# Kernel optimization log

Hardware: AMD Instinct MI355X
Metric: run time of the kernel (lower is better)

## Reference

```python
import jax, jax.numpy as jnp
import numpy as np

N = 50000   # num_nodes
E = 300000  # num_edges
D = 256     # args.dim
F = 1024    # feat_dim
C = 40      # num_labels

def setup_inputs() -> dict:
    key = jax.random.key(0)
    ks = jax.random.split(key, 16)
    def lin(k, fan_in, shape):
        return (jax.random.normal(k, shape, jnp.float32) / np.float32(np.sqrt(fan_in)))
    return {
        "feat": jax.random.normal(ks[0], (N, F), jnp.float32),
        "src": jax.random.randint(ks[1], (E,), 0, N, dtype=jnp.int32),
        "dst": jax.random.randint(ks[2], (E,), 0, N, dtype=jnp.int32),
        "W_fc": lin(ks[3], F, (F, D)), "b_fc": jnp.zeros((D,), jnp.float32),
        "W1": lin(ks[4], D, (D, D)), "b1": jnp.zeros((D,), jnp.float32),
        "W2": lin(ks[5], D, (D, D)), "b2": jnp.zeros((D,), jnp.float32),
        "W3": lin(ks[6], D, (D, D)), "b3": jnp.zeros((D,), jnp.float32),
        "gamma": jnp.ones((D,), jnp.float32), "beta": jnp.zeros((D,), jnp.float32),
        "W_lin": lin(ks[7], D, (D, C)), "b_lin": jnp.zeros((C,), jnp.float32),
    }

def _norms(src, dst, n):
    # DGL GraphConv norm='both': out-degree norm on src side, in-degree on dst side, clamp(min=1)
    ones = jnp.ones(src.shape[0], jnp.float32)
    deg_out = jnp.clip(jax.ops.segment_sum(ones, src, num_segments=n), 1.0)
    deg_in = jnp.clip(jax.ops.segment_sum(ones, dst, num_segments=n), 1.0)
    return deg_out[:, None] ** -0.5, deg_in[:, None] ** -0.5

def _gconv(x, src, dst, norm_s, norm_d, W, b):
    h = x * norm_s                              # [N, D]
    m = jax.ops.segment_sum(h[src], dst, num_segments=x.shape[0])  # SpMM via gather/scatter
    return (m * norm_d) @ W + b

def _bn_elu(x, gamma, beta):
    # training-mode batchnorm math (batch stats, biased var); dropout is identity (eval)
    mu = x.mean(axis=0)
    var = x.var(axis=0)
    y = gamma * (x - mu) * jax.lax.rsqrt(var + 1e-5) + beta
    return jax.nn.elu(y)

def reference(feat, src, dst, W_fc, b_fc, W1, b1, W2, b2, W3, b3, gamma, beta, W_lin, b_lin):
    norm_s, norm_d = _norms(src, dst, feat.shape[0])
    x = feat @ W_fc + b_fc
    x = _gconv(x, src, dst, norm_s, norm_d, W1, b1)
    x = _bn_elu(x, gamma, beta)
    x = _gconv(x, src, dst, norm_s, norm_d, W2, b2)
    x = _bn_elu(x, gamma, beta)
    x = _gconv(x, src, dst, norm_s, norm_d, W3, b3)
    return (x, x @ W_lin + b_lin)
```

## Files before the change

### kernel.cpp

```cpp
#include <hip/hip_runtime.h>

#define N_NODES 50000
#define N_EDGES 300000
#define DIM 256
#define FEAT 1024
#define NCLS 40

typedef unsigned short u16;
typedef __attribute__((ext_vector_type(8))) short short8;
typedef __attribute__((ext_vector_type(4))) float float4v;

__device__ __forceinline__ float bf2f(u16 u) {
  union { float f; unsigned v; } x; x.v = ((unsigned)u) << 16; return x.f;
}
__device__ __forceinline__ u16 f2bf(float f) {
  union { float f; unsigned v; } x; x.f = f;
  unsigned r = 0x7fffu + ((x.v >> 16) & 1u);
  return (u16)((x.v + r) >> 16);
}
__device__ __forceinline__ float flexload(const void* p, size_t i, int f32) {
  return f32 ? ((const float*)p)[i] : bf2f(((const u16*)p)[i]);
}
__device__ __forceinline__ void flexstore(void* p, size_t i, int f32, float v) {
  if (f32) ((float*)p)[i] = v;
  else ((u16*)p)[i] = f2bf(v);
}
__device__ __forceinline__ void async16(const u16* g, u16* l) {
  __builtin_amdgcn_global_load_lds(
      (__attribute__((address_space(1))) void*)g,
      (__attribute__((address_space(3))) void*)l, 16, 0, 0);
}

__global__ __launch_bounds__(256) void k_sniff(const u16* __restrict__ feat,
                                               int* __restrict__ dflag) {
  __shared__ int cnt[256];
  int t = threadIdx.x;
  int ok = 0;
  for (int j = 0; j < 4; ++j) {
    float v = bf2f(feat[(size_t)(t * 4 + j) * 2]);
    float a = fabsf(v);
    if (a < 64.0f && a > 1e-5f) ok++;
  }
  cnt[t] = ok;
  __syncthreads();
  for (int off = 128; off > 0; off >>= 1) {
    if (t < off) cnt[t] += cnt[t + off];
    __syncthreads();
  }
  if (t == 0) dflag[0] = (cnt[0] < 700) ? 1 : 0;
}

__global__ void k_setflag(int* dflag, int v) { dflag[0] = v; }

__global__ void k_filldiag(void* out, int n, float val, const int* __restrict__ dflag) {
  int i = blockIdx.x * blockDim.x + threadIdx.x;
  if (i < n) flexstore(out, i, dflag[0], val);
}

__global__ __launch_bounds__(256) void k_cast(const void* __restrict__ feat,
                                              u16* __restrict__ xf,
                                              const int* __restrict__ dflag) {
  if (dflag[0] == 0) return;
  size_t i = ((size_t)blockIdx.x * 256 + threadIdx.x) * 8;
  const float* f = (const float*)feat;
  float4 a = *(const float4*)&f[i];
  float4 b = *(const float4*)&f[i + 4];
  uint4 o;
  o.x = (unsigned)f2bf(a.x) | ((unsigned)f2bf(a.y) << 16);
  o.y = (unsigned)f2bf(a.z) | ((unsigned)f2bf(a.w) << 16);
  o.z = (unsigned)f2bf(b.x) | ((unsigned)f2bf(b.y) << 16);
  o.w = (unsigned)f2bf(b.z) | ((unsigned)f2bf(b.w) << 16);
  *(uint4*)&xf[i] = o;
}


__global__ void k_zero(unsigned* p, int n) {
  int i = blockIdx.x * blockDim.x + threadIdx.x;
  if (i < n) p[i] = 0u;
}

__global__ void k_deg(const int* __restrict__ src, const int* __restrict__ dst,
                      float* __restrict__ degf, int* __restrict__ degi, int e) {
  int i = blockIdx.x * blockDim.x + threadIdx.x;
  if (i < e) {
    atomicAdd(&degf[src[i]], 1.0f);
    atomicAdd(&degi[dst[i]], 1);
  }
}

__global__ void k_norm(const float* __restrict__ degf, const int* __restrict__ degi,
                       float* __restrict__ ns, float* __restrict__ nd, int n) {
  int i = blockIdx.x * blockDim.x + threadIdx.x;
  if (i < n) {
    ns[i] = rsqrtf(fmaxf(degf[i], 1.0f));
    nd[i] = rsqrtf(fmaxf((float)degi[i], 1.0f));
  }
}

__global__ __launch_bounds__(1024) void k_scan(const int* __restrict__ counts,
                                               int* __restrict__ row_start,
                                               int* __restrict__ cursor, int n) {
  __shared__ int wsum[16];
  __shared__ int carry_s;
  int t = threadIdx.x;
  int lane = t & 63, wv = t >> 6;
  if (t == 0) carry_s = 0;
  __syncthreads();
  for (int base = 0; base < n; base += 4096) {
    int i0 = base + t * 4;
    int v0 = 0, v1 = 0, v2 = 0, v3 = 0;
    if (i0 + 3 < n) {
      int4 c4 = *(const int4*)&counts[i0];
      v0 = c4.x; v1 = c4.y; v2 = c4.z; v3 = c4.w;
    } else {
      if (i0 < n) v0 = counts[i0];
      if (i0 + 1 < n) v1 = counts[i0 + 1];
      if (i0 + 2 < n) v2 = counts[i0 + 2];
      if (i0 + 3 < n) v3 = counts[i0 + 3];
    }
    int s = v0 + v1 + v2 + v3;
    int sc = s;
#pragma unroll
    for (int off = 1; off < 64; off <<= 1) {
      int u = __shfl_up(sc, off, 64);
      if (lane >= off) sc += u;
    }
    if (lane == 63) wsum[wv] = sc;
    __syncthreads();
    if (wv == 0) {
      int w_ = (lane < 16) ? wsum[lane] : 0;
#pragma unroll
      for (int off = 1; off < 16; off <<= 1) {
        int u = __shfl_up(w_, off, 64);
        if (lane >= off) w_ += u;
      }
      if (lane < 16) wsum[lane] = w_;
    }
    __syncthreads();
    int wbase = (wv == 0) ? 0 : wsum[wv - 1];
    int carry = carry_s;
    int excl = carry + wbase + (sc - s);
    if (i0 < n)     { int p = excl;                row_start[i0] = p;     cursor[i0] = p; }
    if (i0 + 1 < n) { int p = excl + v0;           row_start[i0 + 1] = p; cursor[i0 + 1] = p; }
    if (i0 + 2 < n) { int p = excl + v0 + v1;      row_start[i0 + 2] = p; cursor[i0 + 2] = p; }
    if (i0 + 3 < n) { int p = excl + v0 + v1 + v2; row_start[i0 + 3] = p; cursor[i0 + 3] = p; }
    __syncthreads();
    if (t == 1023) carry_s = carry + wbase + sc;
    __syncthreads();
  }
  if (t == 0) row_start[n] = carry_s;
}

__global__ void k_scatter(const int* __restrict__ src, const int* __restrict__ dst,
                          int* __restrict__ cursor, int* __restrict__ csr_src, int e) {
  int i = blockIdx.x * blockDim.x + threadIdx.x;
  if (i < e) {
    int pos = atomicAdd(&cursor[dst[i]], 1);
    csr_src[pos] = src[i];
  }
}

__global__ void k_transpose(const void* __restrict__ w, u16* __restrict__ wt,
                            int K, int Ncols, const int* __restrict__ dflag) {
  int f = dflag[0];
  int i = blockIdx.x * blockDim.x + threadIdx.x;
  if (i < K * Ncols) {
    int k = i / Ncols;
    int c = i - k * Ncols;
    wt[c * K + k] = f2bf(flexload(w, i, f));
  }
}


__global__ __launch_bounds__(256) void k_gemm_a(
    const u16* __restrict__ A0, const u16* __restrict__ A1,
    const u16* __restrict__ Bt, const void* __restrict__ bias,
    void* __restrict__ Cmat, int M, int K, int Nc, int c_flex,
    float* __restrict__ stats, const int* __restrict__ dflag) {
  __shared__ __align__(16) u16 As[64 * 128];
  __shared__ __align__(16) u16 Bs[64 * 128];

  const int f = dflag[0];
  const u16* A = f ? A1 : A0;
  const int cf = c_flex & f;

  const int tid = threadIdx.x;
  const int lane = tid & 63;
  const int wv = tid >> 6;
  const int wm = (wv >> 1) * 64;
  const int wn = (wv & 1) * 64;
  const int quad = lane >> 4;
  const int l15 = lane & 15;
  const int rowBase = blockIdx.x * 128;
  const int colBase = blockIdx.y * 128;

  float4v acc[4][4];
#pragma unroll
  for (int a = 0; a < 4; ++a)
#pragma unroll
    for (int b = 0; b < 4; ++b) {
      acc[a][b][0] = 0.f; acc[a][b][1] = 0.f; acc[a][b][2] = 0.f; acc[a][b][3] = 0.f;
    }

  for (int k0 = 0; k0 < K; k0 += 64) {
    __syncthreads();
#pragma unroll
    for (int r = 0; r < 4; ++r) {
      int j = r * 256 + tid;
      int kq = j >> 7;
      int ml = j & 127;
      int grow = rowBase + ml;
      if (grow >= M) grow = M - 1;
      async16(&A[(size_t)grow * K + k0 + kq * 8], &As[j * 8]);
      async16(&Bt[(size_t)(colBase + ml) * K + k0 + kq * 8], &Bs[j * 8]);
    }
    __syncthreads();
#pragma unroll
    for (int ks = 0; ks < 2; ++ks) {
      short8 afr[4], bfr[4];
#pragma unroll
      for (int t = 0; t < 4; ++t) {
        int kq = ks * 4 + quad;
        afr[t] = *(const short8*)&As[(kq * 128 + wm + t * 16 + l15) * 8];
        bfr[t] = *(const short8*)&Bs[(kq * 128 + wn + t * 16 + l15) * 8];
      }
#pragma unroll
      for (int mt = 0; mt < 4; ++mt)
#pragma unroll
        for (int nt = 0; nt < 4; ++nt)
          acc[mt][nt] = __builtin_amdgcn_mfma_f32_16x16x32_bf16(
              afr[mt], bfr[nt], acc[mt][nt], 0, 0, 0);
    }
  }

#pragma unroll
  for (int nt = 0; nt < 4; ++nt) {
    int col = colBase + wn + nt * 16 + l15;
    float bv = flexload(bias, col, f);
    float s = 0.f, s2 = 0.f;
#pragma unroll
    for (int mt = 0; mt < 4; ++mt) {
#pragma unroll
      for (int r = 0; r < 4; ++r) {
        int row = rowBase + wm + mt * 16 + quad * 4 + r;
        if (row < M) {
          float v = acc[mt][nt][r] + bv;
          if (cf) ((float*)Cmat)[(size_t)row * Nc + col] = v;
          else ((u16*)Cmat)[(size_t)row * Nc + col] = f2bf(v);
          s += v;
          s2 += v * v;
        }
      }
    }
    if (stats) {
      s += __shfl_down(s, 32, 64);
      s += __shfl_down(s, 16, 64);
      s2 += __shfl_down(s2, 32, 64);
      s2 += __shfl_down(s2, 16, 64);
      if (quad == 0) {
        atomicAdd(&stats[col], s);
        atomicAdd(&stats[DIM + col], s2);
      }
    }
  }
}

__global__ __launch_bounds__(256) void k_gemm_flex(
    const void* __restrict__ A, const u16* __restrict__ Bt,
    const void* __restrict__ bias, void* __restrict__ Cmat,
    int M, int K, int Nc, int a_flex, int c_flex,
    const int* __restrict__ dflag) {
  __shared__ __align__(16) u16 As[64 * 128];
  __shared__ __align__(16) u16 Bs[64 * 128];
  const int f = dflag[0];
  const int af = a_flex & f;
  const int cf = c_flex & f;
  const int tid = threadIdx.x;
  const int lane = tid & 63;
  const int wv = tid >> 6;
  const int wm = (wv >> 1) * 64;
  const int wn = (wv & 1) * 64;
  const int quad = lane >> 4;
  const int l15 = lane & 15;
  const int rowBase = blockIdx.x * 128;
  const int colBase = blockIdx.y * 128;
  float4v acc[4][4];
#pragma unroll
  for (int a = 0; a < 4; ++a)
#pragma unroll
    for (int b = 0; b < 4; ++b) {
      acc[a][b][0] = 0.f; acc[a][b][1] = 0.f; acc[a][b][2] = 0.f; acc[a][b][3] = 0.f;
    }
  for (int k0 = 0; k0 < K; k0 += 64) {
    __syncthreads();
#pragma unroll
    for (int r = 0; r < 4; ++r) {
      int j = r * 256 + tid;
      int kq = j >> 7;
      int ml = j & 127;
      int grow = rowBase + ml;
      if (grow >= M) grow = M - 1;
      size_t abase = (size_t)grow * K + k0 + kq * 8;
      if (af) {
        const float* Af = (const float*)A;
        float4 lo = *(const float4*)&Af[abase];
        float4 hi = *(const float4*)&Af[abase + 4];
        u16* d = &As[j * 8];
        d[0] = f2bf(lo.x); d[1] = f2bf(lo.y); d[2] = f2bf(lo.z); d[3] = f2bf(lo.w);
        d[4] = f2bf(hi.x); d[5] = f2bf(hi.y); d[6] = f2bf(hi.z); d[7] = f2bf(hi.w);
      } else {
        const u16* Au = (const u16*)A;
        *(uint4*)&As[j * 8] = *(const uint4*)&Au[abase];
      }
      *(uint4*)&Bs[j * 8] = *(const uint4*)&Bt[(size_t)(colBase + ml) * K + k0 + kq * 8];
    }
    __syncthreads();
#pragma unroll
    for (int ks = 0; ks < 2; ++ks) {
      short8 afr[4], bfr[4];
#pragma unroll
      for (int t = 0; t < 4; ++t) {
        int kq = ks * 4 + quad;
        afr[t] = *(const short8*)&As[(kq * 128 + wm + t * 16 + l15) * 8];
        bfr[t] = *(const short8*)&Bs[(kq * 128 + wn + t * 16 + l15) * 8];
      }
#pragma unroll
      for (int mt = 0; mt < 4; ++mt)
#pragma unroll
        for (int nt = 0; nt < 4; ++nt)
          acc[mt][nt] = __builtin_amdgcn_mfma_f32_16x16x32_bf16(
              afr[mt], bfr[nt], acc[mt][nt], 0, 0, 0);
    }
  }
#pragma unroll
  for (int nt = 0; nt < 4; ++nt) {
    int col = colBase + wn + nt * 16 + l15;
    float bv = flexload(bias, col, f);
#pragma unroll
    for (int mt = 0; mt < 4; ++mt) {
#pragma unroll
      for (int r = 0; r < 4; ++r) {
        int row = rowBase + wm + mt * 16 + quad * 4 + r;
        if (row < M) {
          float v = acc[mt][nt][r] + bv;
          if (cf) ((float*)Cmat)[(size_t)row * Nc + col] = v;
          else ((u16*)Cmat)[(size_t)row * Nc + col] = f2bf(v);
        }
      }
    }
  }
}


__global__ __launch_bounds__(256) void k_spmm(
    const u16* __restrict__ x, u16* __restrict__ y,
    const int* __restrict__ row_start, const int* __restrict__ csr_src,
    const float* __restrict__ ns, const float* __restrict__ nd, int n) {
  int wid = (blockIdx.x * blockDim.x + threadIdx.x) >> 6;
  int lane = threadIdx.x & 63;
  if (wid >= n) return;
  int e0 = row_start[wid];
  int e1 = row_start[wid + 1];
  int c = lane * 4;
  float a0 = 0.f, a1 = 0.f, a2 = 0.f, a3 = 0.f;
  for (int e = e0; e < e1; ++e) {
    int s = csr_src[e];
    float w = ns[s];
    uint2 v = *(const uint2*)&x[(size_t)s * DIM + c];
    a0 += w * bf2f((u16)(v.x & 0xffffu));
    a1 += w * bf2f((u16)(v.x >> 16));
    a2 += w * bf2f((u16)(v.y & 0xffffu));
    a3 += w * bf2f((u16)(v.y >> 16));
  }
  float wd = nd[wid];
  uint2 o;
  o.x = (unsigned)f2bf(a0 * wd) | ((unsigned)f2bf(a1 * wd) << 16);
  o.y = (unsigned)f2bf(a2 * wd) | ((unsigned)f2bf(a3 * wd) << 16);
  *(uint2*)&y[(size_t)wid * DIM + c] = o;
}


__global__ __launch_bounds__(256) void k_bnfin(const float* __restrict__ stats,
                                               const void* __restrict__ gamma,
                                               const void* __restrict__ beta,
                                               float* __restrict__ gb, int nrows,
                                               const int* __restrict__ dflag) {
  int f = dflag[0];
  int t = threadIdx.x;
  float inv_n = 1.0f / (float)nrows;
  float mu = stats[t] * inv_n;
  float var = stats[DIM + t] * inv_n - mu * mu;
  float rs = rsqrtf(var + 1e-5f);
  float g = flexload(gamma, t, f) * rs;
  float b = flexload(beta, t, f) - mu * g;
  gb[t] = g;
  gb[DIM + t] = b;
}

__global__ __launch_bounds__(256) void k_bnapply(u16* __restrict__ x,
                                                 const float* __restrict__ gb, int nrows) {
  int t = threadIdx.x;
  float g = gb[t];
  float b = gb[DIM + t];
  for (int r = blockIdx.x; r < nrows; r += gridDim.x) {
    size_t idx = (size_t)r * DIM + t;
    float y = g * bf2f(x[idx]) + b;
    y = y > 0.f ? y : expm1f(y);
    x[idx] = f2bf(y);
  }
}


__global__ __launch_bounds__(256) void k_final(const void* __restrict__ x,
                                               const void* __restrict__ W,
                                               const void* __restrict__ bias,
                                               void* __restrict__ out, int nrows,
                                               const int* __restrict__ dflag) {
  __shared__ u16 xs[64 * DIM];
  __shared__ u16 wl[DIM * NCLS];
  int f = dflag[0];
  int t = threadIdx.x;
  int rowBase = blockIdx.x * 64;
  for (int i = t; i < 64 * DIM; i += 256) {
    int r = rowBase + (i >> 8);
    if (r >= nrows) r = nrows - 1;
    xs[i] = f2bf(flexload(x, (size_t)r * DIM + (i & 255), f));
  }
  for (int i = t; i < DIM * NCLS; i += 256) wl[i] = f2bf(flexload(W, i, f));
  __syncthreads();
  for (int o = t; o < 64 * NCLS; o += 256) {
    int r = o / NCLS;
    int c = o - r * NCLS;
    float acc = 0.f;
    const u16* xr = &xs[r * DIM];
#pragma unroll 8
    for (int k = 0; k < DIM; ++k) acc += bf2f(xr[k]) * bf2f(wl[k * NCLS + c]);
    int grow = rowBase + r;
    if (grow < nrows)
      flexstore(out, (size_t)N_NODES * DIM + (size_t)grow * NCLS + c, f,
                acc + flexload(bias, c, f));
  }
}


extern "C" void kernel_launch(void* const* d_in, const int* in_sizes, int n_in,
                              void* d_out, int out_size, void* d_ws, size_t ws_size,
                              hipStream_t stream) {
  static const int EXP[15] = {51200000, 300000, 300000, 262144, 256, 65536, 256,
                              65536, 256, 65536, 256, 256, 256, 10240, 40};
  bool ok_sizes = (n_in == 15);
  if (ok_sizes)
    for (int i = 0; i < 15; ++i)
      if (in_sizes[i] != EXP[i]) ok_sizes = false;

  char* w = (char*)d_ws;
  size_t o = 0;
  auto take = [&](size_t bytes) {
    size_t r = o;
    o += (bytes + 255) & ~(size_t)255;
    return r;
  };
  size_t o_degf = take(N_NODES * 4);
  size_t o_degi = take(N_NODES * 4);
  size_t o_stat = take(1024 * 4);
  size_t zero_bytes = o;
  size_t o_flag = take(256);
  size_t o_gb = take(512 * 4);
  size_t o_ns = take(N_NODES * 4);
  size_t o_nd = take(N_NODES * 4);
  size_t o_rs = take((N_NODES + 1) * 4);
  size_t o_cur = take(N_NODES * 4);
  size_t o_csr = take(N_EDGES * 4);
  size_t o_wfc = take((size_t)FEAT * DIM * 2);
  size_t o_w1 = take(DIM * DIM * 2);
  size_t o_w2 = take(DIM * DIM * 2);
  size_t o_w3 = take(DIM * DIM * 2);
  size_t o_xa = take((size_t)N_NODES * DIM * 2);
  size_t required = o;
  size_t o_xf = take((size_t)N_NODES * FEAT * 2);
  size_t required_xf = o;
  bool have_xf = ws_size >= required_xf;

  if (!ok_sizes || ws_size < required) {
    int* dflag0 = (int*)d_ws;
    float val = ok_sizes ? 1.0f : 2.0f;
    if (n_in > 0 && in_sizes[0] >= 2048)
      k_sniff<<<1, 256, 0, stream>>>((const u16*)d_in[0], dflag0);
    else
      k_setflag<<<1, 1, 0, stream>>>(dflag0, 0);
    k_filldiag<<<(out_size + 255) / 256, 256, 0, stream>>>(d_out, out_size, val, dflag0);
    return;
  }

  const void* feat = d_in[0];
  const int* src = (const int*)d_in[1];
  const int* dst = (const int*)d_in[2];
  const void* W_fc = d_in[3];
  const void* b_fc = d_in[4];
  const void* W1 = d_in[5];
  const void* b1 = d_in[6];
  const void* W2 = d_in[7];
  const void* b2 = d_in[8];
  const void* W3 = d_in[9];
  const void* b3 = d_in[10];
  const void* gamma = d_in[11];
  const void* beta = d_in[12];
  const void* W_lin = d_in[13];
  const void* b_lin = d_in[14];

  float* degf = (float*)(w + o_degf);
  int* degi = (int*)(w + o_degi);
  float* stats = (float*)(w + o_stat);
  int* dflag = (int*)(w + o_flag);
  float* gb = (float*)(w + o_gb);
  float* norm_s = (float*)(w + o_ns);
  float* norm_d = (float*)(w + o_nd);
  int* row_start = (int*)(w + o_rs);
  int* cursor = (int*)(w + o_cur);
  int* csr_src = (int*)(w + o_csr);
  u16* WtFc = (u16*)(w + o_wfc);
  u16* Wt1 = (u16*)(w + o_w1);
  u16* Wt2 = (u16*)(w + o_w2);
  u16* Wt3 = (u16*)(w + o_w3);
  u16* xA = (u16*)(w + o_xa);
  u16* xF = (u16*)(w + o_xf);

  u16* ping = (u16*)d_out;

  k_sniff<<<1, 256, 0, stream>>>((const u16*)feat, dflag);

  int zero_words = (int)(zero_bytes / 4);
  k_zero<<<(zero_words + 255) / 256, 256, 0, stream>>>((unsigned*)(w + 0), zero_words);
  k_deg<<<(N_EDGES + 255) / 256, 256, 0, stream>>>(src, dst, degf, degi, N_EDGES);
  k_norm<<<(N_NODES + 255) / 256, 256, 0, stream>>>(degf, degi, norm_s, norm_d, N_NODES);
  k_scan<<<1, 1024, 0, stream>>>(degi, row_start, cursor, N_NODES);
  k_scatter<<<(N_EDGES + 255) / 256, 256, 0, stream>>>(src, dst, cursor, csr_src, N_EDGES);
  k_transpose<<<((FEAT * DIM) + 255) / 256, 256, 0, stream>>>(W_fc, WtFc, FEAT, DIM, dflag);
  k_transpose<<<((DIM * DIM) + 255) / 256, 256, 0, stream>>>(W1, Wt1, DIM, DIM, dflag);
  k_transpose<<<((DIM * DIM) + 255) / 256, 256, 0, stream>>>(W2, Wt2, DIM, DIM, dflag);
  k_transpose<<<((DIM * DIM) + 255) / 256, 256, 0, stream>>>(W3, Wt3, DIM, DIM, dflag);

  dim3 gg((N_NODES + 127) / 128, DIM / 128);

  if (have_xf) {
    k_cast<<<(N_NODES * FEAT) / (256 * 8), 256, 0, stream>>>(feat, xF, dflag);
    k_gemm_a<<<gg, 256, 0, stream>>>((const u16*)feat, xF, WtFc, b_fc, ping,
                                     N_NODES, FEAT, DIM, 0, (float*)nullptr, dflag);
  } else {
    k_gemm_flex<<<gg, 256, 0, stream>>>(feat, WtFc, b_fc, ping,
                                        N_NODES, FEAT, DIM, 1, 0, dflag);
  }

  k_spmm<<<(N_NODES + 3) / 4, 256, 0, stream>>>(ping, xA, row_start, csr_src, norm_s, norm_d, N_NODES);
  k_gemm_a<<<gg, 256, 0, stream>>>(xA, xA, Wt1, b1, ping, N_NODES, DIM, DIM, 0, stats, dflag);
  k_bnfin<<<1, 256, 0, stream>>>(stats, gamma, beta, gb, N_NODES, dflag);
  k_bnapply<<<512, 256, 0, stream>>>(ping, gb, N_NODES);

  k_spmm<<<(N_NODES + 3) / 4, 256, 0, stream>>>(ping, xA, row_start, csr_src, norm_s, norm_d, N_NODES);
  k_gemm_a<<<gg, 256, 0, stream>>>(xA, xA, Wt2, b2, ping, N_NODES, DIM, DIM, 0, stats + 512, dflag);
  k_bnfin<<<1, 256, 0, stream>>>(stats + 512, gamma, beta, gb, N_NODES, dflag);
  k_bnapply<<<512, 256, 0, stream>>>(ping, gb, N_NODES);

  k_spmm<<<(N_NODES + 3) / 4, 256, 0, stream>>>(ping, xA, row_start, csr_src, norm_s, norm_d, N_NODES);
  k_gemm_a<<<gg, 256, 0, stream>>>(xA, xA, Wt3, b3, d_out, N_NODES, DIM, DIM, 1, (float*)nullptr, dflag);

  k_final<<<(N_NODES + 63) / 64, 256, 0, stream>>>(d_out, W_lin, b_lin, d_out, N_NODES, dflag);
}
```

Before: 1.010 ms.

## Fuse input cast into FC GEMM, fold BN-ELU into SpMM, precompose logits weights

Replaces the separate fp32-to-bf16 cast pass and tiled FC GEMM with one full-width kernel that loads fp32 features into LDS and converts them while building MFMA fragments. Folds the batchnorm+ELU apply into the next SpMM's gather, so the in-place normalise pass over activations goes away. Precomputes W3·W_lin and the combined bias, then computes logits with an MFMA kernel straight from the aggregated features instead of the scalar final kernel. In exchange, ELU is recomputed per gathered edge, rounding changes because the composed weight is stored in bf16, and the FC kernel uses more LDS and registers.

```diff
diff --git a/kernel.cpp b/kernel.cpp
--- a/kernel.cpp
+++ b/kernel.cpp
@@ -1,10 +1,12 @@
 #include <hip/hip_runtime.h>
+#include <hip/hip_bf16.h>
 
 #define N_NODES 50000
 #define N_EDGES 300000
 #define DIM 256
 #define FEAT 1024
 #define NCLS 40
+#define WPAD 264
 
 typedef unsigned short u16;
 typedef __attribute__((ext_vector_type(8))) short short8;
@@ -18,6 +20,11 @@
   unsigned r = 0x7fffu + ((x.v >> 16) & 1u);
   return (u16)((x.v + r) >> 16);
 }
+__device__ __forceinline__ unsigned pk2(float a, float b) {
+  union { __hip_bfloat162 h; unsigned u; } cv;
+  cv.h = __float22bfloat162_rn(make_float2(a, b));
+  return cv.u;
+}
 __device__ __forceinline__ float flexload(const void* p, size_t i, int f32) {
   return f32 ? ((const float*)p)[i] : bf2f(((const u16*)p)[i]);
 }
@@ -25,7 +32,7 @@
   if (f32) ((float*)p)[i] = v;
   else ((u16*)p)[i] = f2bf(v);
 }
-__device__ __forceinline__ void async16(const u16* g, u16* l) {
+__device__ __forceinline__ void async16(const void* g, void* l) {
   __builtin_amdgcn_global_load_lds(
       (__attribute__((address_space(1))) void*)g,
       (__attribute__((address_space(3))) void*)l, 16, 0, 0);
@@ -55,22 +62,6 @@
 __global__ void k_filldiag(void* out, int n, float val, const int* __restrict__ dflag) {
   int i = blockIdx.x * blockDim.x + threadIdx.x;
   if (i < n) flexstore(out, i, dflag[0], val);
-}
-
-__global__ __launch_bounds__(256) void k_cast(const void* __restrict__ feat,
-                                              u16* __restrict__ xf,
-                                              const int* __restrict__ dflag) {
-  if (dflag[0] == 0) return;
-  size_t i = ((size_t)blockIdx.x * 256 + threadIdx.x) * 8;
-  const float* f = (const float*)feat;
-  float4 a = *(const float4*)&f[i];
-  float4 b = *(const float4*)&f[i + 4];
-  uint4 o;
-  o.x = (unsigned)f2bf(a.x) | ((unsigned)f2bf(a.y) << 16);
-  o.y = (unsigned)f2bf(a.z) | ((unsigned)f2bf(a.w) << 16);
-  o.z = (unsigned)f2bf(b.x) | ((unsigned)f2bf(b.y) << 16);
-  o.w = (unsigned)f2bf(b.z) | ((unsigned)f2bf(b.w) << 16);
-  *(uint4*)&xf[i] = o;
 }
 
 
@@ -171,17 +162,147 @@
   }
 }
 
+__global__ __launch_bounds__(256) void k_combo(const void* __restrict__ W3,
+                                               const void* __restrict__ Wlin,
+                                               u16* __restrict__ Wct,
+                                               const int* __restrict__ dflag) {
+  int f = dflag[0];
+  int c = blockIdx.x;
+  int k = threadIdx.x;
+  float acc = 0.f;
+  if (c < NCLS)
+    for (int n = 0; n < DIM; ++n)
+      acc += flexload(W3, (size_t)k * DIM + n, f) * flexload(Wlin, (size_t)n * NCLS + c, f);
+  Wct[c * WPAD + k] = f2bf(acc);
+}
+
+__global__ void k_combobias(const void* __restrict__ b3, const void* __restrict__ Wlin,
+                            const void* __restrict__ blin, float* __restrict__ bcb,
+                            const int* __restrict__ dflag) {
+  int f = dflag[0];
+  int c = threadIdx.x;
+  if (c >= NCLS) return;
+  float acc = flexload(blin, c, f);
+  for (int n = 0; n < DIM; ++n)
+    acc += flexload(b3, n, f) * flexload(Wlin, (size_t)n * NCLS + c, f);
+  bcb[c] = acc;
+}
+
+
+__global__ __launch_bounds__(256) void k_gemm_fc(
+    const void* __restrict__ A, const u16* __restrict__ Bt,
+    const void* __restrict__ bias, u16* __restrict__ Cmat,
+    int M, const int* __restrict__ dflag) {
+  __shared__ __align__(16) u16 lds_[32768];
+  u16* Bs = lds_;
+  u16* Asb = lds_ + 16384;
+  float* Asf = (float*)(lds_ + 16384);
+
+  const int f = dflag[0];
+  const int tid = threadIdx.x;
+  const int lane = tid & 63;
+  const int wv = tid >> 6;
+  const int wm = (wv >> 1) * 64;
+  const int wn = (wv & 1) * 128;
+  const int quad = lane >> 4;
+  const int l15 = lane & 15;
+  const int rowBase = blockIdx.x * 128;
+
+  float4v acc[4][8];
+#pragma unroll
+  for (int a = 0; a < 4; ++a)
+#pragma unroll
+    for (int b = 0; b < 8; ++b) {
+      acc[a][b][0] = 0.f; acc[a][b][1] = 0.f; acc[a][b][2] = 0.f; acc[a][b][3] = 0.f;
+    }
+
+  for (int k0 = 0; k0 < FEAT; k0 += 64) {
+    __syncthreads();
+#pragma unroll
+    for (int r = 0; r < 8; ++r) {
+      int j = r * 256 + tid;
+      int kq = j >> 8, n = j & 255;
+      async16(&Bt[(size_t)n * FEAT + k0 + kq * 8], &Bs[(size_t)j * 8]);
+    }
+    if (f) {
+      const float* Af = (const float*)A;
+#pragma unroll
+      for (int r = 0; r < 8; ++r) {
+        int j = r * 256 + tid;
+        int kq = j >> 8, m = (j & 255) >> 1, half = j & 1;
+        int grow = rowBase + m;
+        if (grow >= M) grow = M - 1;
+        async16(&Af[(size_t)grow * FEAT + k0 + kq * 8 + half * 4], &Asf[(size_t)j * 4]);
+      }
+    } else {
+      const u16* Au = (const u16*)A;
+#pragma unroll
+      for (int r = 0; r < 4; ++r) {
+        int j = r * 256 + tid;
+        int kq = j >> 7, m = j & 127;
+        int grow = rowBase + m;
+        if (grow >= M) grow = M - 1;
+        async16(&Au[(size_t)grow * FEAT + k0 + kq * 8], &Asb[(size_t)j * 8]);
+      }
+    }
+    __syncthreads();
+#pragma unroll
+    for (int ks = 0; ks < 2; ++ks) {
+      int kq = ks * 4 + quad;
+      short8 afr[4], bfr[8];
+      if (f) {
+#pragma unroll
+        for (int t = 0; t < 4; ++t) {
+          int row = wm + t * 16 + l15;
+          float4 lo = *(const float4*)&Asf[(size_t)((kq * 128 + row) * 2 + 0) * 4];
+          float4 hi = *(const float4*)&Asf[(size_t)((kq * 128 + row) * 2 + 1) * 4];
+          union { short8 s; unsigned u[4]; } o;
+          o.u[0] = pk2(lo.x, lo.y); o.u[1] = pk2(lo.z, lo.w);
+          o.u[2] = pk2(hi.x, hi.y); o.u[3] = pk2(hi.z, hi.w);
+          afr[t] = o.s;
+        }
+      } else {
+#pragma unroll
+        for (int t = 0; t < 4; ++t)
+          afr[t] = *(const short8*)&Asb[(size_t)(kq * 128 + wm + t * 16 + l15) * 8];
+      }
+#pragma unroll
+      for (int t = 0; t < 8; ++t)
+        bfr[t] = *(const short8*)&Bs[(size_t)(kq * 256 + wn + t * 16 + l15) * 8];
+#pragma unroll
+      for (int mt = 0; mt < 4; ++mt)
+#pragma unroll
+        for (int nt = 0; nt < 8; ++nt)
+          acc[mt][nt] = __builtin_amdgcn_mfma_f32_16x16x32_bf16(
+              afr[mt], bfr[nt], acc[mt][nt], 0, 0, 0);
+    }
+  }
+
+#pragma unroll
+  for (int nt = 0; nt < 8; ++nt) {
+    int col = wn + nt * 16 + l15;
+    float bv = flexload(bias, col, f);
+#pragma unroll
+    for (int mt = 0; mt < 4; ++mt) {
+#pragma unroll
+      for (int r = 0; r < 4; ++r) {
+        int row = rowBase + wm + mt * 16 + quad * 4 + r;
+        if (row < M) Cmat[(size_t)row * DIM + col] = f2bf(acc[mt][nt][r] + bv);
+      }
+    }
+  }
+}
+
 
 __global__ __launch_bounds__(256) void k_gemm_a(
-    const u16* __restrict__ A0, const u16* __restrict__ A1,
-    const u16* __restrict__ Bt, const void* __restrict__ bias,
-    void* __restrict__ Cmat, int M, int K, int Nc, int c_flex,
-    float* __restrict__ stats, const int* __restrict__ dflag) {
+    const u16* __restrict__ A, const u16* __restrict__ Bt,
+    const void* __restrict__ bias, void* __restrict__ Cmat,
+    int M, int K, int Nc, int c_flex, float* __restrict__ stats,
+    const int* __restrict__ dflag) {
   __shared__ __align__(16) u16 As[64 * 128];
   __shared__ __align__(16) u16 Bs[64 * 128];
 
   const int f = dflag[0];
-  const u16* A = f ? A1 : A0;
   const int cf = c_flex & f;
 
   const int tid = threadIdx.x;
@@ -211,8 +332,8 @@
       int ml = j & 127;
       int grow = rowBase + ml;
       if (grow >= M) grow = M - 1;
-      async16(&A[(size_t)grow * K + k0 + kq * 8], &As[j * 8]);
-      async16(&Bt[(size_t)(colBase + ml) * K + k0 + kq * 8], &Bs[j * 8]);
+      async16(&A[(size_t)grow * K + k0 + kq * 8], &As[(size_t)j * 8]);
+      async16(&Bt[(size_t)(colBase + ml) * K + k0 + kq * 8], &Bs[(size_t)j * 8]);
     }
     __syncthreads();
 #pragma unroll
@@ -221,8 +342,8 @@
 #pragma unroll
       for (int t = 0; t < 4; ++t) {
         int kq = ks * 4 + quad;
-        afr[t] = *(const short8*)&As[(kq * 128 + wm + t * 16 + l15) * 8];
-        bfr[t] = *(const short8*)&Bs[(kq * 128 + wn + t * 16 + l15) * 8];
+        afr[t] = *(const short8*)&As[(size_t)(kq * 128 + wm + t * 16 + l15) * 8];
+        bfr[t] = *(const short8*)&Bs[(size_t)(kq * 128 + wn + t * 16 + l15) * 8];
       }
 #pragma unroll
       for (int mt = 0; mt < 4; ++mt)
@@ -265,97 +386,12 @@
   }
 }
 
-__global__ __launch_bounds__(256) void k_gemm_flex(
-    const void* __restrict__ A, const u16* __restrict__ Bt,
-    const void* __restrict__ bias, void* __restrict__ Cmat,
-    int M, int K, int Nc, int a_flex, int c_flex,
-    const int* __restrict__ dflag) {
-  __shared__ __align__(16) u16 As[64 * 128];
-  __shared__ __align__(16) u16 Bs[64 * 128];
-  const int f = dflag[0];
-  const int af = a_flex & f;
-  const int cf = c_flex & f;
-  const int tid = threadIdx.x;
-  const int lane = tid & 63;
-  const int wv = tid >> 6;
-  const int wm = (wv >> 1) * 64;
-  const int wn = (wv & 1) * 64;
-  const int quad = lane >> 4;
-  const int l15 = lane & 15;
-  const int rowBase = blockIdx.x * 128;
-  const int colBase = blockIdx.y * 128;
-  float4v acc[4][4];
-#pragma unroll
-  for (int a = 0; a < 4; ++a)
-#pragma unroll
-    for (int b = 0; b < 4; ++b) {
-      acc[a][b][0] = 0.f; acc[a][b][1] = 0.f; acc[a][b][2] = 0.f; acc[a][b][3] = 0.f;
-    }
-  for (int k0 = 0; k0 < K; k0 += 64) {
-    __syncthreads();
-#pragma unroll
-    for (int r = 0; r < 4; ++r) {
-      int j = r * 256 + tid;
-      int kq = j >> 7;
-      int ml = j & 127;
-      int grow = rowBase + ml;
-      if (grow >= M) grow = M - 1;
-      size_t abase = (size_t)grow * K + k0 + kq * 8;
-      if (af) {
-        const float* Af = (const float*)A;
-        float4 lo = *(const float4*)&Af[abase];
-        float4 hi = *(const float4*)&Af[abase + 4];
-        u16* d = &As[j * 8];
-        d[0] = f2bf(lo.x); d[1] = f2bf(lo.y); d[2] = f2bf(lo.z); d[3] = f2bf(lo.w);
-        d[4] = f2bf(hi.x); d[5] = f2bf(hi.y); d[6] = f2bf(hi.z); d[7] = f2bf(hi.w);
-      } else {
-        const u16* Au = (const u16*)A;
-        *(uint4*)&As[j * 8] = *(const uint4*)&Au[abase];
-      }
-      *(uint4*)&Bs[j * 8] = *(const uint4*)&Bt[(size_t)(colBase + ml) * K + k0 + kq * 8];
-    }
-    __syncthreads();
-#pragma unroll
-    for (int ks = 0; ks < 2; ++ks) {
-      short8 afr[4], bfr[4];
-#pragma unroll
-      for (int t = 0; t < 4; ++t) {
-        int kq = ks * 4 + quad;
-        afr[t] = *(const short8*)&As[(kq * 128 + wm + t * 16 + l15) * 8];
-        bfr[t] = *(const short8*)&Bs[(kq * 128 + wn + t * 16 + l15) * 8];
-      }
-#pragma unroll
-      for (int mt = 0; mt < 4; ++mt)
-#pragma unroll
-        for (int nt = 0; nt < 4; ++nt)
-          acc[mt][nt] = __builtin_amdgcn_mfma_f32_16x16x32_bf16(
-              afr[mt], bfr[nt], acc[mt][nt], 0, 0, 0);
-    }
-  }
-#pragma unroll
-  for (int nt = 0; nt < 4; ++nt) {
-    int col = colBase + wn + nt * 16 + l15;
-    float bv = flexload(bias, col, f);
-#pragma unroll
-    for (int mt = 0; mt < 4; ++mt) {
-#pragma unroll
-      for (int r = 0; r < 4; ++r) {
-        int row = rowBase + wm + mt * 16 + quad * 4 + r;
-        if (row < M) {
-          float v = acc[mt][nt][r] + bv;
-          if (cf) ((float*)Cmat)[(size_t)row * Nc + col] = v;
-          else ((u16*)Cmat)[(size_t)row * Nc + col] = f2bf(v);
-        }
-      }
-    }
-  }
-}
-
 
 __global__ __launch_bounds__(256) void k_spmm(
     const u16* __restrict__ x, u16* __restrict__ y,
     const int* __restrict__ row_start, const int* __restrict__ csr_src,
-    const float* __restrict__ ns, const float* __restrict__ nd, int n) {
+    const float* __restrict__ ns, const float* __restrict__ nd,
+    const float* __restrict__ gb, int n) {
   int wid = (blockIdx.x * blockDim.x + threadIdx.x) >> 6;
   int lane = threadIdx.x & 63;
   if (wid >= n) return;
@@ -363,14 +399,33 @@
   int e1 = row_start[wid + 1];
   int c = lane * 4;
   float a0 = 0.f, a1 = 0.f, a2 = 0.f, a3 = 0.f;
-  for (int e = e0; e < e1; ++e) {
-    int s = csr_src[e];
-    float w = ns[s];
-    uint2 v = *(const uint2*)&x[(size_t)s * DIM + c];
-    a0 += w * bf2f((u16)(v.x & 0xffffu));
-    a1 += w * bf2f((u16)(v.x >> 16));
-    a2 += w * bf2f((u16)(v.y & 0xffffu));
-    a3 += w * bf2f((u16)(v.y >> 16));
+  if (gb) {
+    float g0 = gb[c], g1 = gb[c + 1], g2 = gb[c + 2], g3 = gb[c + 3];
+    float b0 = gb[DIM + c], b1 = gb[DIM + c + 1], b2 = gb[DIM + c + 2], b3 = gb[DIM + c + 3];
+    for (int e = e0; e < e1; ++e) {
+      int s = csr_src[e];
+      float w = ns[s];
+      uint2 v = *(const uint2*)&x[(size_t)s * DIM + c];
+      float x0 = g0 * bf2f((u16)(v.x & 0xffffu)) + b0;
+      float x1 = g1 * bf2f((u16)(v.x >> 16)) + b1;
+      float x2 = g2 * bf2f((u16)(v.y & 0xffffu)) + b2;
+      float x3 = g3 * bf2f((u16)(v.y >> 16)) + b3;
+      x0 = x0 > 0.f ? x0 : expm1f(x0);
+      x1 = x1 > 0.f ? x1 : expm1f(x1);
+      x2 = x2 > 0.f ? x2 : expm1f(x2);
+      x3 = x3 > 0.f ? x3 : expm1f(x3);
+      a0 += w * x0; a1 += w * x1; a2 += w * x2; a3 += w * x3;
+    }
+  } else {
+    for (int e = e0; e < e1; ++e) {
+      int s = csr_src[e];
+      float w = ns[s];
+      uint2 v = *(const uint2*)&x[(size_t)s * DIM + c];
+      a0 += w * bf2f((u16)(v.x & 0xffffu));
+      a1 += w * bf2f((u16)(v.x >> 16));
+      a2 += w * bf2f((u16)(v.y & 0xffffu));
+      a3 += w * bf2f((u16)(v.y >> 16));
+    }
   }
   float wd = nd[wid];
   uint2 o;
@@ -397,48 +452,73 @@
   gb[DIM + t] = b;
 }
 
-__global__ __launch_bounds__(256) void k_bnapply(u16* __restrict__ x,
-                                                 const float* __restrict__ gb, int nrows) {
-  int t = threadIdx.x;
-  float g = gb[t];
-  float b = gb[DIM + t];
-  for (int r = blockIdx.x; r < nrows; r += gridDim.x) {
-    size_t idx = (size_t)r * DIM + t;
-    float y = g * bf2f(x[idx]) + b;
-    y = y > 0.f ? y : expm1f(y);
-    x[idx] = f2bf(y);
-  }
-}
-
-
-__global__ __launch_bounds__(256) void k_final(const void* __restrict__ x,
-                                               const void* __restrict__ W,
-                                               const void* __restrict__ bias,
-                                               void* __restrict__ out, int nrows,
-                                               const int* __restrict__ dflag) {
-  __shared__ u16 xs[64 * DIM];
-  __shared__ u16 wl[DIM * NCLS];
-  int f = dflag[0];
-  int t = threadIdx.x;
-  int rowBase = blockIdx.x * 64;
-  for (int i = t; i < 64 * DIM; i += 256) {
-    int r = rowBase + (i >> 8);
-    if (r >= nrows) r = nrows - 1;
-    xs[i] = f2bf(flexload(x, (size_t)r * DIM + (i & 255), f));
-  }
-  for (int i = t; i < DIM * NCLS; i += 256) wl[i] = f2bf(flexload(W, i, f));
-  __syncthreads();
-  for (int o = t; o < 64 * NCLS; o += 256) {
-    int r = o / NCLS;
-    int c = o - r * NCLS;
-    float acc = 0.f;
-    const u16* xr = &xs[r * DIM];
-#pragma unroll 8
-    for (int k = 0; k < DIM; ++k) acc += bf2f(xr[k]) * bf2f(wl[k * NCLS + c]);
-    int grow = rowBase + r;
-    if (grow < nrows)
-      flexstore(out, (size_t)N_NODES * DIM + (size_t)grow * NCLS + c, f,
-                acc + flexload(bias, c, f));
+
+__global__ __launch_bounds__(256) void k_logits(
+    const u16* __restrict__ A, const u16* __restrict__ Wct,
+    const float* __restrict__ bcb, void* __restrict__ out,
+    int M, const int* __restrict__ dflag) {
+  __shared__ __align__(16) u16 As[64 * 128];
+  __shared__ __align__(16) u16 Wl[48 * WPAD];
+  const int f = dflag[0];
+  const int tid = threadIdx.x;
+  const int lane = tid & 63, wv = tid >> 6;
+  const int quad = lane >> 4, l15 = lane & 15;
+  const int rowBase = blockIdx.x * 128;
+
+  for (int i = tid; i < 48 * WPAD / 2; i += 256)
+    ((unsigned*)Wl)[i] = ((const unsigned*)Wct)[i];
+
+  float4v acc[2][3];
+#pragma unroll
+  for (int a = 0; a < 2; ++a)
+#pragma unroll
+    for (int b = 0; b < 3; ++b) {
+      acc[a][b][0] = 0.f; acc[a][b][1] = 0.f; acc[a][b][2] = 0.f; acc[a][b][3] = 0.f;
+    }
+
+  for (int k0 = 0; k0 < DIM; k0 += 64) {
+    __syncthreads();
+#pragma unroll
+    for (int r = 0; r < 4; ++r) {
+      int j = r * 256 + tid;
+      int kq = j >> 7, m = j & 127;
+      int grow = rowBase + m;
+      if (grow >= M) grow = M - 1;
+      async16(&A[(size_t)grow * DIM + k0 + kq * 8], &As[(size_t)j * 8]);
+    }
+    __syncthreads();
+#pragma unroll
+    for (int ks = 0; ks < 2; ++ks) {
+      int kq = ks * 4 + quad;
+      short8 afr[2], bfr[3];
+#pragma unroll
+      for (int t = 0; t < 2; ++t)
+        afr[t] = *(const short8*)&As[(size_t)(kq * 128 + wv * 32 + t * 16 + l15) * 8];
+#pragma unroll
+      for (int t = 0; t < 3; ++t)
+        bfr[t] = *(const short8*)&Wl[(size_t)(t * 16 + l15) * WPAD + k0 + kq * 8];
+#pragma unroll
+      for (int mt = 0; mt < 2; ++mt)
+#pragma unroll
+        for (int nt = 0; nt < 3; ++nt)
+          acc[mt][nt] = __builtin_amdgcn_mfma_f32_16x16x32_bf16(
+              afr[mt], bfr[nt], acc[mt][nt], 0, 0, 0);
+    }
+  }
+
+#pragma unroll
+  for (int nt = 0; nt < 3; ++nt) {
+    int col = nt * 16 + l15;
+    float bv = (col < NCLS) ? bcb[col] : 0.f;
+#pragma unroll
+    for (int mt = 0; mt < 2; ++mt) {
+#pragma unroll
+      for (int r = 0; r < 4; ++r) {
+        int row = rowBase + wv * 32 + mt * 16 + quad * 4 + r;
+        if (row < M && col < NCLS)
+          flexstore(out, (size_t)N_NODES * DIM + (size_t)row * NCLS + col, f, acc[mt][nt][r] + bv);
+      }
+    }
   }
 }
 
@@ -475,11 +555,10 @@
   size_t o_w1 = take(DIM * DIM * 2);
   size_t o_w2 = take(DIM * DIM * 2);
   size_t o_w3 = take(DIM * DIM * 2);
+  size_t o_wc = take(48 * WPAD * 2);
+  size_t o_bc = take(NCLS * 4);
   size_t o_xa = take((size_t)N_NODES * DIM * 2);
   size_t required = o;
-  size_t o_xf = take((size_t)N_NODES * FEAT * 2);
-  size_t required_xf = o;
-  bool have_xf = ws_size >= required_xf;
 
   if (!ok_sizes || ws_size < required) {
     int* dflag0 = (int*)d_ws;
@@ -522,8 +601,9 @@
   u16* Wt1 = (u16*)(w + o_w1);
   u16* Wt2 = (u16*)(w + o_w2);
   u16* Wt3 = (u16*)(w + o_w3);
+  u16* Wct = (u16*)(w + o_wc);
+  float* bcb = (float*)(w + o_bc);
   u16* xA = (u16*)(w + o_xa);
-  u16* xF = (u16*)(w + o_xf);
 
   u16* ping = (u16*)d_out;
 
@@ -539,30 +619,24 @@
   k_transpose<<<((DIM * DIM) + 255) / 256, 256, 0, stream>>>(W1, Wt1, DIM, DIM, dflag);
   k_transpose<<<((DIM * DIM) + 255) / 256, 256, 0, stream>>>(W2, Wt2, DIM, DIM, dflag);
   k_transpose<<<((DIM * DIM) + 255) / 256, 256, 0, stream>>>(W3, Wt3, DIM, DIM, dflag);
+  k_combo<<<48, 256, 0, stream>>>(W3, W_lin, Wct, dflag);
+  k_combobias<<<1, 64, 0, stream>>>(b3, W_lin, b_lin, bcb, dflag);
 
   dim3 gg((N_NODES + 127) / 128, DIM / 128);
-
-  if (have_xf) {
-    k_cast<<<(N_NODES * FEAT) / (256 * 8), 256, 0, stream>>>(feat, xF, dflag);
-    k_gemm_a<<<gg, 256, 0, stream>>>((const u16*)feat, xF, WtFc, b_fc, ping,
-                                     N_NODES, FEAT, DIM, 0, (float*)nullptr, dflag);
-  } else {
-    k_gemm_flex<<<gg, 256, 0, stream>>>(feat, WtFc, b_fc, ping,
-                                        N_NODES, FEAT, DIM, 1, 0, dflag);
-  }
-
-  k_spmm<<<(N_NODES + 3) / 4, 256, 0, stream>>>(ping, xA, row_start, csr_src, norm_s, norm_d, N_NODES);
-  k_gemm_a<<<gg, 256, 0, stream>>>(xA, xA, Wt1, b1, ping, N_NODES, DIM, DIM, 0, stats, dflag);
+  int gfc = (N_NODES + 127) / 128;
+
+  k_gemm_fc<<<gfc, 256, 0, stream>>>(feat, WtFc, b_fc, ping, N_NODES, dflag);
+
+  k_spmm<<<(N_NODES + 3) / 4, 256, 0, stream>>>(ping, xA, row_start, csr_src, norm_s, norm_d, (const float*)nullptr, N_NODES);
+  k_gemm_a<<<gg, 256, 0, stream>>>(xA, Wt1, b1, ping, N_NODES, DIM, DIM, 0, stats, dflag);
   k_bnfin<<<1, 256, 0, stream>>>(stats, gamma, beta, gb, N_NODES, dflag);
-  k_bnapply<<<512, 256, 0, stream>>>(ping, gb, N_NODES);
-
-  k_spmm<<<(N_NODES + 3) / 4, 256, 0, stream>>>(ping, xA, row_start, csr_src, norm_s, norm_d, N_NODES);
-  k_gemm_a<<<gg, 256, 0, stream>>>(xA, xA, Wt2, b2, ping, N_NODES, DIM, DIM, 0, stats + 512, dflag);
+
+  k_spmm<<<(N_NODES + 3) / 4, 256, 0, stream>>>(ping, xA, row_start, csr_src, norm_s, norm_d, gb, N_NODES);
+  k_gemm_a<<<gg, 256, 0, stream>>>(xA, Wt2, b2, ping, N_NODES, DIM, DIM, 0, stats + 512, dflag);
   k_bnfin<<<1, 256, 0, stream>>>(stats + 512, gamma, beta, gb, N_NODES, dflag);
-  k_bnapply<<<512, 256, 0, stream>>>(ping, gb, N_NODES);
-
-  k_spmm<<<(N_NODES + 3) / 4, 256, 0, stream>>>(ping, xA, row_start, csr_src, norm_s, norm_d, N_NODES);
-  k_gemm_a<<<gg, 256, 0, stream>>>(xA, xA, Wt3, b3, d_out, N_NODES, DIM, DIM, 1, (float*)nullptr, dflag);
-
-  k_final<<<(N_NODES + 63) / 64, 256, 0, stream>>>(d_out, W_lin, b_lin, d_out, N_NODES, dflag);
-}
+
+  k_spmm<<<(N_NODES + 3) / 4, 256, 0, stream>>>(ping, xA, row_start, csr_src, norm_s, norm_d, gb, N_NODES);
+  k_gemm_a<<<gg, 256, 0, stream>>>(xA, Wt3, b3, d_out, N_NODES, DIM, DIM, 1, (float*)nullptr, dflag);
+
+  k_logits<<<gfc, 256, 0, stream>>>(xA, Wct, bcb, d_out, N_NODES, dflag);
+}
```

New measurement: 933.0 us. -7.6%, faster.
